# Kernel tuning notes

Hardware: AMD Instinct MI355X
Metric: run time of the kernel (lower is better)

## Reference

```python
import jax, jax.numpy as jnp
import numpy as np

L, H, D_MODEL, FFN = 2, 8, 1024, 4096
HD = D_MODEL // H          # head size = 128
SCALE_BASE = 512           # XPOS scale_base
EPS = 1e-5                 # LayerNorm / GroupNorm eps (torch default)


def _layernorm(x, w, b):
    mu = x.mean(-1, keepdims=True)
    var = ((x - mu) ** 2).mean(-1, keepdims=True)
    return (x - mu) * jax.lax.rsqrt(var + EPS) * w + b


def _groupnorm(y, w, b):
    # GroupNorm(heads, v_dim) applied row-wise on (B*S, v_dim): normalize each head's HD slice.
    B, S, _ = y.shape
    yg = y.reshape(B, S, H, HD)
    mu = yg.mean(-1, keepdims=True)
    var = ((yg - mu) ** 2).mean(-1, keepdims=True)
    yn = ((yg - mu) * jax.lax.rsqrt(var + EPS)).reshape(B, S, H * HD)
    return yn * w + b


def _xpos_tables(S):
    # XPOS: scale = ((arange(0,HD,2)+0.4*HD)/(1.4*HD)) ** (pos/scale_base); sin/cos from fixed_pos_embedding(scale)
    scale_vec = (np.arange(0, HD, 2) + 0.4 * HD) / (1.4 * HD)            # (HD/2,)
    power = (np.arange(S, dtype=np.float64) / SCALE_BASE)[:, None]
    scale = scale_vec[None, :] ** power                                   # (S, HD/2)
    half = HD // 2
    inv_freq = 1.0 / (10000.0 ** (np.arange(half, dtype=np.float64) / half))
    ang = np.arange(S, dtype=np.float64)[:, None] * inv_freq[None, :]
    sin, cos = np.sin(ang), np.cos(ang)
    dup = lambda m: jnp.asarray(np.repeat(m, 2, axis=-1).astype(np.float32))  # duplicate_interleave -> (S, HD)
    return dup(sin * scale), dup(cos * scale), dup(sin / scale), dup(cos / scale)


def _rotate_every_two(x):
    x1, x2 = x[..., ::2], x[..., 1::2]
    return jnp.stack((-x2, x1), axis=-1).reshape(x.shape)


def _decay_mask(S):
    # gammas = 1 - exp(linspace(log(1/32), log(1/512), H)); D[h,n,m] = gamma_h^(n-m) * (n>=m)
    gammas = 1.0 - np.exp(np.linspace(np.log(1.0 / 32), np.log(1.0 / 512), H))
    n = np.arange(S)[:, None]
    m = np.arange(S)[None, :]
    diff = (n - m).astype(np.float64)
    D = np.where(n >= m, gammas[:, None, None] ** diff[None], 0.0)
    return jnp.asarray(D.astype(np.float32))  # (H, S, S)


def setup_inputs() -> dict:
    key = jax.random.key(0)
    ks = jax.random.split(key, 8)
    B, S = 2, 2048
    rn = lambda k, shape, s: jax.random.normal(k, shape, dtype=jnp.float32) * s
    return {
        "X": rn(ks[0], (B, S, D_MODEL), 1.0),
        "ln1_w": jnp.ones((L, D_MODEL), jnp.float32), "ln1_b": jnp.zeros((L, D_MODEL), jnp.float32),
        "ln2_w": jnp.ones((L, D_MODEL), jnp.float32), "ln2_b": jnp.zeros((L, D_MODEL), jnp.float32),
        "WQ": rn(ks[1], (L, H, D_MODEL, HD), 1.0 / D_MODEL),
        "WK": rn(ks[2], (L, H, D_MODEL, HD), 1.0 / D_MODEL),
        "WV": rn(ks[3], (L, H, D_MODEL, HD), 1.0 / D_MODEL),
        "gn_w": jnp.ones((L, D_MODEL), jnp.float32), "gn_b": jnp.zeros((L, D_MODEL), jnp.float32),
        "WG": rn(ks[4], (L, D_MODEL, D_MODEL), 1.0 / D_MODEL),
        "WO": rn(ks[5], (L, D_MODEL, D_MODEL), 1.0 / D_MODEL),
        "ffn_w1": rn(ks[6], (L, D_MODEL, FFN), 1.0 / np.sqrt(D_MODEL)),
        "ffn_b1": jnp.zeros((L, FFN), jnp.float32),
        "ffn_w2": rn(ks[7], (L, FFN, D_MODEL), 1.0 / np.sqrt(FFN)),
        "ffn_b2": jnp.zeros((L, D_MODEL), jnp.float32),
    }


def reference(X, ln1_w, ln1_b, ln2_w, ln2_b, WQ, WK, WV, gn_w, gn_b, WG, WO,
              ffn_w1, ffn_b1, ffn_w2, ffn_b2):
    B, S, _ = X.shape
    sinq, cosq, sink, cosk = _xpos_tables(S)   # (S, HD) each; K uses downscale (1/scale)
    Dm = _decay_mask(S)                         # (H, S, S)
    for i in range(L):
        Xn = _layernorm(X, ln1_w[i], ln1_b[i])
        Q = jnp.einsum('bsd,hdk->bhsk', Xn, WQ[i])
        K = jnp.einsum('bsd,hdk->bhsk', Xn, WK[i])
        V = jnp.einsum('bsd,hdk->bhsk', Xn, WV[i])
        Q = Q * cosq + _rotate_every_two(Q) * sinq
        K = K * cosk + _rotate_every_two(K) * sink
        scores = jnp.einsum('bhsk,bhtk->bhst', Q, K) * Dm[None]  # decay-masked retention
        Yh = jnp.einsum('bhst,bhtk->bhsk', scores, V)
        Y = Yh.transpose(0, 2, 1, 3).reshape(B, S, H * HD)        # concat heads
        Y = _groupnorm(Y, gn_w[i], gn_b[i])
        G = jax.nn.silu(Xn @ WG[i])                               # swish gate on layernormed input
        Y = (G * Y) @ WO[i] + X                                   # retention + residual
        Yn = _layernorm(Y, ln2_w[i], ln2_b[i])
        X = jax.nn.silu(Yn @ ffn_w1[i] + ffn_b1[i]) @ ffn_w2[i] + ffn_b2[i] + Y
    return X
```

## Files before the change

kernel.cpp:

```cpp
#include <hip/hip_runtime.h>
#include <cstdint>
#include <cstddef>

#define LN_ 2
#define HH 8
#define DM 1024
#define FFN_ 4096
#define HDD 128
#define SS 2048
#define BB 2
#define RR (BB*SS)

typedef __bf16 bf16x8 __attribute__((ext_vector_type(8)));
typedef __bf16 bf16x4 __attribute__((ext_vector_type(4)));
typedef __bf16 bf16x2 __attribute__((ext_vector_type(2)));
typedef float  f32x4  __attribute__((ext_vector_type(4)));

__device__ __forceinline__ float silu_f(float x) { return x / (1.0f + expf(-x)); }

__device__ __forceinline__ void glds16(const void* g, void* l) {
  __builtin_amdgcn_global_load_lds(
      (const __attribute__((address_space(1))) unsigned int*)g,
      (__attribute__((address_space(3))) unsigned int*)l, 16, 0, 0);
}


__global__ void init_tables_k(float* __restrict__ sq, float* __restrict__ cq,
                              float* __restrict__ sk, float* __restrict__ ck,
                              float* __restrict__ lg2g) {
  int s = blockIdx.x, k = threadIdx.x;
  int j = k >> 1;
  double sv    = (2.0 * j + 0.4 * HDD) / (1.4 * HDD);
  double p     = (double)s / 512.0;
  double scale = pow(sv, p);
  double invf  = pow(10000.0, -((double)j) / 64.0);
  double ang   = (double)s * invf;
  double sn = sin(ang), cs = cos(ang);
  size_t idx = (size_t)s * HDD + k;
  sq[idx] = (float)(sn * scale);
  cq[idx] = (float)(cs * scale);
  sk[idx] = (float)(sn / scale);
  ck[idx] = (float)(cs / scale);
  if (s == 0 && k < HH) {
    double a0 = log(1.0 / 32.0), a1 = log(1.0 / 512.0);
    double x = a0 + (a1 - a0) * ((double)k / 7.0);
    lg2g[k] = (float)(log(1.0 - exp(x)) / log(2.0));
  }
}

__global__ __launch_bounds__(256) void ln_pack_k(
    const float* __restrict__ X, const float* __restrict__ w,
    const float* __restrict__ b, char* __restrict__ ph, char* __restrict__ pl) {
  const int row = blockIdx.x, tid = threadIdx.x;
  const float* x = X + (size_t)row * DM;
  float4 v = *(const float4*)(x + tid * 4);
  float s = v.x + v.y + v.z + v.w;
  float q = v.x * v.x + v.y * v.y + v.z * v.z + v.w * v.w;
#pragma unroll
  for (int o = 32; o > 0; o >>= 1) { s += __shfl_xor(s, o); q += __shfl_xor(q, o); }
  __shared__ float ss[4], qq[4];
  if ((tid & 63) == 0) { ss[tid >> 6] = s; qq[tid >> 6] = q; }
  __syncthreads();
  float S  = ss[0] + ss[1] + ss[2] + ss[3];
  float Qs = qq[0] + qq[1] + qq[2] + qq[3];
  float mu  = S * (1.0f / DM);
  float var = Qs * (1.0f / DM) - mu * mu;
  float rs  = 1.0f / sqrtf(var + 1e-5f);
  float4 wv = *(const float4*)(w + tid * 4);
  float4 bv = *(const float4*)(b + tid * 4);
  float y[4];
  y[0] = (v.x - mu) * rs * wv.x + bv.x;
  y[1] = (v.y - mu) * rs * wv.y + bv.y;
  y[2] = (v.z - mu) * rs * wv.z + bv.z;
  y[3] = (v.w - mu) * rs * wv.w + bv.w;
  bf16x4 hv, lv;
#pragma unroll
  for (int r = 0; r < 4; ++r) {
    __bf16 h = (__bf16)y[r];
    hv[r] = h;
    lv[r] = (__bf16)(y[r] - (float)h);
  }
  size_t tb = ((size_t)(row >> 7) * (DM / 64) + (tid >> 4)) * 16384;
  int off = (row & 127) * 128 + (((tid & 15) * 8) ^ ((row & 7) << 4));
  *(bf16x4*)(ph + tb + off) = hv;
  *(bf16x4*)(pl + tb + off) = lv;
}

__global__ __launch_bounds__(256) void packw_k(
    const float* __restrict__ W, char* __restrict__ dh, char* __restrict__ dl,
    int N, int qkv) {
  const int tn = blockIdx.x, tk = blockIdx.y, nkt = gridDim.y;
  __shared__ float L[64][132];
  const int k0 = tk * 64;
  const size_t srcbase = qkv ? ((size_t)tn * 131072 + (size_t)k0 * 128)
                             : ((size_t)k0 * N + (size_t)tn * 128);
  const int rstr = qkv ? 128 : N;
#pragma unroll
  for (int it = 0; it < 8; ++it) {
    int q = threadIdx.x + it * 256;
    int kk = q >> 5, c4 = (q & 31) * 4;
    float4 v = *(const float4*)(W + srcbase + (size_t)kk * rstr + c4);
    *(float4*)&L[kk][c4] = v;
  }
  __syncthreads();
  const size_t tb = ((size_t)tn * nkt + tk) * 16384;
#pragma unroll
  for (int it = 0; it < 4; ++it) {
    int o = threadIdx.x + it * 256;
    int n = o >> 3, k8 = o & 7;
    bf16x8 hv, lv;
#pragma unroll
    for (int j = 0; j < 8; ++j) {
      float x = L[k8 * 8 + j][n];
      __bf16 h = (__bf16)x;
      hv[j] = h;
      lv[j] = (__bf16)(x - (float)h);
    }
    int off = n * 128 + ((k8 * 16) ^ ((n & 7) << 4));
    *(bf16x8*)(dh + tb + off) = hv;
    *(bf16x8*)(dl + tb + off) = lv;
  }
}

__global__ __launch_bounds__(256) void vtpack_k(
    const float* __restrict__ V, char* __restrict__ dh, char* __restrict__ dl) {
  const int st = blockIdx.x, bh = blockIdx.y;
  __shared__ float L[64][132];
  const float* src = V + ((size_t)bh * SS + st * 64) * HDD;
#pragma unroll
  for (int it = 0; it < 8; ++it) {
    int q = threadIdx.x + it * 256;
    int r = q >> 5, c4 = (q & 31) * 4;
    *(float4*)&L[r][c4] = *(const float4*)(src + (size_t)r * HDD + c4);
  }
  __syncthreads();
  const size_t tb = ((size_t)bh * 32 + st) * 16384;
#pragma unroll
  for (int it = 0; it < 4; ++it) {
    int o = threadIdx.x + it * 256;
    int d = o >> 3, s8 = o & 7;
    bf16x8 hv, lv;
#pragma unroll
    for (int j = 0; j < 8; ++j) {
      float x = L[s8 * 8 + j][d];
      __bf16 h = (__bf16)x;
      hv[j] = h;
      lv[j] = (__bf16)(x - (float)h);
    }
    int off = d * 128 + ((s8 * 16) ^ ((d & 7) << 4));
    *(bf16x8*)(dh + tb + off) = hv;
    *(bf16x8*)(dl + tb + off) = lv;
  }
}

template <int MODE>
__global__ __launch_bounds__(256, 1) void mgemm_k(
    const char* __restrict__ pAh, const char* __restrict__ pAl,
    const char* __restrict__ pBh, const char* __restrict__ pBl,
    float* __restrict__ C, const float* __restrict__ bias,
    const float* __restrict__ resid, char* __restrict__ outH,
    char* __restrict__ outL, const float* __restrict__ tsin,
    const float* __restrict__ tcos, int M, int N, int K) {
  __shared__ char lds[2][4][16384];
  const int tid = threadIdx.x, lane = tid & 63, w = tid >> 6;
  const int wm = w & 1, wn = w >> 1;
  const int bx = blockIdx.x, by = blockIdx.y;
  const int nkt = K >> 6;
  const size_t tileA0 = (size_t)by * nkt * 16384;
  const size_t tileB0 = (size_t)bx * nkt * 16384;
  const int swz = (lane & 7) << 4;
  const int l15 = lane & 15, l4 = lane >> 4;

  f32x4 acc[4][4];
#pragma unroll
  for (int i = 0; i < 4; ++i)
#pragma unroll
    for (int j = 0; j < 4; ++j) acc[i][j] = (f32x4){0.f, 0.f, 0.f, 0.f};

  auto stage = [&](int buf, int t) {
    const size_t oA = tileA0 + (size_t)t * 16384;
    const size_t oB = tileB0 + (size_t)t * 16384;
#pragma unroll
    for (int c = 0; c < 4; ++c) {
      const size_t go = (size_t)c * 4096 + w * 1024 + lane * 16;
      const int lo = c * 4096 + w * 1024;
      glds16(pAh + oA + go, &lds[buf][0][lo]);
      glds16(pAl + oA + go, &lds[buf][1][lo]);
      glds16(pBh + oB + go, &lds[buf][2][lo]);
      glds16(pBl + oB + go, &lds[buf][3][lo]);
    }
  };

  auto comp = [&](int buf) {
#pragma unroll
    for (int ks = 0; ks < 2; ++ks) {
      const int kb = ks * 64 + l4 * 16;
      bf16x8 amh[4], aml[4], anh[4], anl[4];
#pragma unroll
      for (int f = 0; f < 4; ++f) {
        const int rm = wm * 64 + f * 16 + l15;
        const int ra = rm * 128 + (kb ^ swz);
        amh[f] = *(const bf16x8*)&lds[buf][0][ra];
        aml[f] = *(const bf16x8*)&lds[buf][1][ra];
        const int rn = wn * 64 + f * 16 + l15;
        const int rb = rn * 128 + (kb ^ swz);
        anh[f] = *(const bf16x8*)&lds[buf][2][rb];
        anl[f] = *(const bf16x8*)&lds[buf][3][rb];
      }
#pragma unroll
      for (int nf = 0; nf < 4; ++nf)
#pragma unroll
        for (int mf = 0; mf < 4; ++mf) {
          acc[nf][mf] = __builtin_amdgcn_mfma_f32_16x16x32_bf16(
              anh[nf], amh[mf], acc[nf][mf], 0, 0, 0);
          acc[nf][mf] = __builtin_amdgcn_mfma_f32_16x16x32_bf16(
              anh[nf], aml[mf], acc[nf][mf], 0, 0, 0);
          acc[nf][mf] = __builtin_amdgcn_mfma_f32_16x16x32_bf16(
              anl[nf], amh[mf], acc[nf][mf], 0, 0, 0);
        }
    }
  };

  stage(0, 0);
  __syncthreads();
  int buf = 0;
  for (int t = 0; t < nkt - 1; ++t) {
    stage(buf ^ 1, t + 1);
    comp(buf);
    __syncthreads();
    buf ^= 1;
  }
  comp(buf);

  const int mBase = by * 128 + wm * 64 + l15;
  const int nBase = bx * 128 + wn * 64 + l4 * 4;
#pragma unroll
  for (int nf = 0; nf < 4; ++nf)
#pragma unroll
    for (int mf = 0; mf < 4; ++mf) {
      const int m = mBase + mf * 16;
      const int n = nBase + nf * 16;
      f32x4 v = acc[nf][mf];
      if (MODE == 0) {
        *(f32x4*)(C + (((size_t)(m >> 11) * HH + (n >> 7)) * SS + (m & (SS - 1)))
                          * HDD + (n & (HDD - 1))) = v;
      } else if (MODE == 1) {
#pragma unroll
        for (int r = 0; r < 4; ++r) v[r] = silu_f(v[r]);
        *(f32x4*)(C + (size_t)m * N + n) = v;
      } else if (MODE == 2) {
        f32x4 rz = *(const f32x4*)(resid + (size_t)m * N + n);
        v += rz;
        *(f32x4*)(C + (size_t)m * N + n) = v;
      } else if (MODE == 3) {
        f32x4 bz = *(const f32x4*)(bias + n);
        bf16x4 hv, lv;
#pragma unroll
        for (int r = 0; r < 4; ++r) {
          float y = silu_f(v[r] + bz[r]);
          __bf16 h = (__bf16)y;
          hv[r] = h;
          lv[r] = (__bf16)(y - (float)h);
        }
        size_t tb = ((size_t)(m >> 7) * (N >> 6) + (n >> 6)) * 16384;
        int off = (m & 127) * 128 + (((n & 63) * 2) ^ ((m & 7) << 4));
        *(bf16x4*)(outH + tb + off) = hv;
        *(bf16x4*)(outL + tb + off) = lv;
      } else if (MODE == 4) {
        f32x4 bz = *(const f32x4*)(bias + n);
        f32x4 rz = *(const f32x4*)(resid + (size_t)m * N + n);
        v += bz + rz;
        *(f32x4*)(C + (size_t)m * N + n) = v;
      } else {
        int s = m & (SS - 1);
        int d = n & (HDD - 1);
        f32x4 sn = *(const f32x4*)(tsin + (size_t)s * HDD + d);
        f32x4 cn = *(const f32x4*)(tcos + (size_t)s * HDD + d);
        float o0 = v[0] * cn[0] - v[1] * sn[0];
        float o1 = v[1] * cn[1] + v[0] * sn[1];
        float o2 = v[2] * cn[2] - v[3] * sn[2];
        float o3 = v[3] * cn[3] + v[2] * sn[3];
        float oo[4] = {o0, o1, o2, o3};
        bf16x4 hv, lv;
#pragma unroll
        for (int r = 0; r < 4; ++r) {
          __bf16 h = (__bf16)oo[r];
          hv[r] = h;
          lv[r] = (__bf16)(oo[r] - (float)h);
        }
        size_t tile = ((size_t)(m >> 11) * HH + (n >> 7)) * 32 + (s >> 7) * 2 + (d >> 6);
        size_t off = tile * 16384 + (s & 127) * 128 + (((d & 63) * 2) ^ ((s & 7) << 4));
        *(bf16x4*)(outH + off) = hv;
        *(bf16x4*)(outL + off) = lv;
      }
    }
}

__global__ __launch_bounds__(256, 2) void mattn_k(
    const char* __restrict__ pQh, const char* __restrict__ pQl,
    const char* __restrict__ pKh, const char* __restrict__ pKl,
    const char* __restrict__ pVh, const char* __restrict__ pVl,
    const float* __restrict__ lg2g, float* __restrict__ Y) {
  __shared__ char Kls[2][2][8192];
  __shared__ char Vls[2][16384];
  __shared__ char Pls[2][8192];
  const int qt = 31 - blockIdx.x;
  const int bh = blockIdx.y;
  const int tid = threadIdx.x, lane = tid & 63, w = tid >> 6;
  const int wn = w & 1, wq = w >> 1;
  const int l15 = lane & 15, lg = lane >> 4;
  const float lg2 = lg2g[bh & 7];
  const size_t tb0 = (size_t)bh * 32;
  const int n0 = qt * 64;
  const int nt = qt + 1;

  bf16x8 qh[2][4], ql[2][4];
#pragma unroll
  for (int nf = 0; nf < 2; ++nf) {
    int rr = n0 + wn * 32 + nf * 16 + l15;
    size_t rowbase = (tb0 + (size_t)(rr >> 7) * 2) * 16384 + (size_t)(rr & 127) * 128;
    int sw = (rr & 7) << 4;
#pragma unroll
    for (int ks = 0; ks < 4; ++ks) {
      int d = ks * 32 + lg * 8;
      size_t a = rowbase + (size_t)(d >> 6) * 16384 + (((d & 63) * 2) ^ sw);
      qh[nf][ks] = *(const bf16x8*)(pQh + a);
      ql[nf][ks] = *(const bf16x8*)(pQl + a);
    }
  }

  f32x4 yacc[2][4];
#pragma unroll
  for (int i = 0; i < 2; ++i)
#pragma unroll
    for (int j = 0; j < 4; ++j) yacc[i][j] = (f32x4){0.f, 0.f, 0.f, 0.f};

  auto stageK = [&](int mt) {
    size_t half = (size_t)(mt & 1) * 8192;
#pragma unroll
    for (int dt = 0; dt < 2; ++dt) {
      size_t tile = (tb0 + (size_t)(mt >> 1) * 2 + dt) * 16384 + half;
#pragma unroll
      for (int c = 0; c < 2; ++c) {
        size_t go = (size_t)c * 4096 + w * 1024 + lane * 16;
        glds16(pKh + tile + go, &Kls[dt][0][c * 4096 + w * 1024]);
        glds16(pKl + tile + go, &Kls[dt][1][c * 4096 + w * 1024]);
      }
    }
  };
  auto stageV = [&](int mt) {
    size_t tile = (tb0 + mt) * 16384;
#pragma unroll
    for (int c = 0; c < 4; ++c) {
      size_t go = (size_t)c * 4096 + w * 1024 + lane * 16;
      glds16(pVh + tile + go, &Vls[0][c * 4096 + w * 1024]);
      glds16(pVl + tile + go, &Vls[1][c * 4096 + w * 1024]);
    }
  };

  stageK(0);
  stageV(0);
  __syncthreads();

  for (int mt = 0; mt < nt; ++mt) {
    f32x4 sacc[2][2];
#pragma unroll
    for (int i = 0; i < 2; ++i)
#pragma unroll
      for (int j = 0; j < 2; ++j) sacc[i][j] = (f32x4){0.f, 0.f, 0.f, 0.f};
#pragma unroll
    for (int ks = 0; ks < 4; ++ks) {
      int d = ks * 32 + lg * 8;
      bf16x8 kh[2], kl[2];
#pragma unroll
      for (int mf = 0; mf < 2; ++mf) {
        int m = wq * 32 + mf * 16 + l15;
        int off = (m & 63) * 128 + (((d & 63) * 2) ^ ((m & 7) << 4));
        kh[mf] = *(const bf16x8*)&Kls[d >> 6][0][off];
        kl[mf] = *(const bf16x8*)&Kls[d >> 6][1][off];
      }
#pragma unroll
      for (int nf = 0; nf < 2; ++nf)
#pragma unroll
        for (int mf = 0; mf < 2; ++mf) {
          sacc[nf][mf] = __builtin_amdgcn_mfma_f32_16x16x32_bf16(
              qh[nf][ks], kh[mf], sacc[nf][mf], 0, 0, 0);
          sacc[nf][mf] = __builtin_amdgcn_mfma_f32_16x16x32_bf16(
              qh[nf][ks], kl[mf], sacc[nf][mf], 0, 0, 0);
          sacc[nf][mf] = __builtin_amdgcn_mfma_f32_16x16x32_bf16(
              ql[nf][ks], kh[mf], sacc[nf][mf], 0, 0, 0);
        }
    }
    asm volatile("s_barrier" ::: "memory");
    if (mt + 1 < nt) stageK(mt + 1);

#pragma unroll
    for (int nf = 0; nf < 2; ++nf)
#pragma unroll
      for (int mf = 0; mf < 2; ++mf)
#pragma unroll
        for (int r = 0; r < 4; ++r) {
          int nl = wn * 32 + nf * 16 + lg * 4 + r;
          int ml = wq * 32 + mf * 16 + l15;
          int diff = (n0 + nl) - (mt * 64 + ml);
          float dec = (diff >= 0) ? exp2f((float)diff * lg2) : 0.0f;
          float p = sacc[nf][mf][r] * dec;
          __bf16 h = (__bf16)p;
          int off = nl * 128 + ((ml * 2) ^ ((nl & 7) << 4));
          *(__bf16*)&Pls[0][off] = h;
          *(__bf16*)&Pls[1][off] = (__bf16)(p - (float)h);
        }
    asm volatile("s_waitcnt lgkmcnt(0)" ::: "memory");
    asm volatile("s_barrier" ::: "memory");

#pragma unroll
    for (int ks = 0; ks < 2; ++ks) {
      int mchunk = ks * 32 + lg * 8;
      bf16x8 ph[2], pl2[2], vh[4], vl2[4];
#pragma unroll
      for (int nf = 0; nf < 2; ++nf) {
        int nl = wn * 32 + nf * 16 + l15;
        int off = nl * 128 + ((mchunk * 2) ^ ((nl & 7) << 4));
        ph[nf]  = *(const bf16x8*)&Pls[0][off];
        pl2[nf] = *(const bf16x8*)&Pls[1][off];
      }
#pragma unroll
      for (int df = 0; df < 4; ++df) {
        int d = wq * 64 + df * 16 + l15;
        int off = d * 128 + ((mchunk * 2) ^ ((d & 7) << 4));
        vh[df]  = *(const bf16x8*)&Vls[0][off];
        vl2[df] = *(const bf16x8*)&Vls[1][off];
      }
#pragma unroll
      for (int nf = 0; nf < 2; ++nf)
#pragma unroll
        for (int df = 0; df < 4; ++df) {
          yacc[nf][df] = __builtin_amdgcn_mfma_f32_16x16x32_bf16(
              ph[nf], vh[df], yacc[nf][df], 0, 0, 0);
          yacc[nf][df] = __builtin_amdgcn_mfma_f32_16x16x32_bf16(
              ph[nf], vl2[df], yacc[nf][df], 0, 0, 0);
          yacc[nf][df] = __builtin_amdgcn_mfma_f32_16x16x32_bf16(
              pl2[nf], vh[df], yacc[nf][df], 0, 0, 0);
        }
    }
    asm volatile("s_barrier" ::: "memory");
    if (mt + 1 < nt) stageV(mt + 1);
    __syncthreads();
  }

  const size_t yrow0 = (size_t)(bh >> 3) * SS + n0;
  const int hcol = (bh & 7) * HDD;
#pragma unroll
  for (int nf = 0; nf < 2; ++nf)
#pragma unroll
    for (int df = 0; df < 4; ++df)
#pragma unroll
      for (int r = 0; r < 4; ++r) {
        int nl = wn * 32 + nf * 16 + lg * 4 + r;
        int d  = wq * 64 + df * 16 + l15;
        Y[(yrow0 + nl) * DM + hcol + d] = yacc[nf][df][r];
      }
}

__global__ __launch_bounds__(256) void gn_gate_k(
    const float* __restrict__ Y, const float* __restrict__ w,
    const float* __restrict__ b, const float* __restrict__ G,
    char* __restrict__ ph, char* __restrict__ pl) {
  int g    = blockIdx.x * 4 + (threadIdx.x >> 6);
  int lane = threadIdx.x & 63;
  float2 v = *(const float2*)(Y + (size_t)g * HDD + lane * 2);
  float s = v.x + v.y, q = v.x * v.x + v.y * v.y;
#pragma unroll
  for (int o = 32; o > 0; o >>= 1) { s += __shfl_xor(s, o); q += __shfl_xor(q, o); }
  float mu  = s * (1.0f / HDD);
  float var = q * (1.0f / HDD) - mu * mu;
  float rs  = 1.0f / sqrtf(var + 1e-5f);
  int m   = g >> 3;
  int col = (g & 7) * HDD + lane * 2;
  float2 wv = *(const float2*)(w + col);
  float2 bv = *(const float2*)(b + col);
  float2 gv = *(const float2*)(G + (size_t)g * HDD + lane * 2);
  float ox = ((v.x - mu) * rs * wv.x + bv.x) * gv.x;
  float oy = ((v.y - mu) * rs * wv.y + bv.y) * gv.y;
  __bf16 hx = (__bf16)ox, hy = (__bf16)oy;
  bf16x2 hv, lv;
  hv[0] = hx; hv[1] = hy;
  lv[0] = (__bf16)(ox - (float)hx); lv[1] = (__bf16)(oy - (float)hy);
  size_t tb = ((size_t)(m >> 7) * (DM / 64) + (col >> 6)) * 16384;
  int off = (m & 127) * 128 + (((col & 63) * 2) ^ ((m & 7) << 4));
  *(bf16x2*)(ph + tb + off) = hv;
  *(bf16x2*)(pl + tb + off) = lv;
}

extern "C" void kernel_launch(void* const* d_in, const int* in_sizes, int n_in,
                              void* d_out, int out_size, void* d_ws, size_t ws_size,
                              hipStream_t stream) {
  (void)in_sizes; (void)n_in; (void)out_size; (void)ws_size;
  const float* X0   = (const float*)d_in[0];
  const float* ln1w = (const float*)d_in[1];
  const float* ln1b = (const float*)d_in[2];
  const float* ln2w = (const float*)d_in[3];
  const float* ln2b = (const float*)d_in[4];
  const float* WQ   = (const float*)d_in[5];
  const float* WK   = (const float*)d_in[6];
  const float* WV   = (const float*)d_in[7];
  const float* gnw  = (const float*)d_in[8];
  const float* gnb  = (const float*)d_in[9];
  const float* WG   = (const float*)d_in[10];
  const float* WO   = (const float*)d_in[11];
  const float* W1   = (const float*)d_in[12];
  const float* B1   = (const float*)d_in[13];
  const float* W2   = (const float*)d_in[14];
  const float* B2   = (const float*)d_in[15];

  char* wsb = (char*)d_ws;
  const size_t MB = 1 << 20;
  float* bufA = (float*)(wsb + 0 * MB);
  float* bufB = (float*)(wsb + 16 * MB);
  float* bufE = (float*)(wsb + 32 * MB);
  float* bufF = (float*)(wsb + 48 * MB);
  float* bufG = (float*)(wsb + 64 * MB);
  float* sq   = (float*)(wsb + 80 * MB);
  float* cq   = (float*)(wsb + 81 * MB);
  float* sk   = (float*)(wsb + 82 * MB);
  float* ck   = (float*)(wsb + 83 * MB);
  float* lg2g = (float*)(wsb + 84 * MB);
  char* pXh = wsb + 85 * MB;
  char* pXl = wsb + 93 * MB;
  char* pWh = wsb + 101 * MB;
  char* pWl = wsb + 127 * MB;
  char* R   = wsb + 153 * MB;
  char* pFh = R;
  char* pFl = R + 32 * MB;
  char* pQh = R;
  char* pQl = R + 8 * MB;
  char* pKh = R + 16 * MB;
  char* pKl = R + 24 * MB;
  char* pVh = R + 32 * MB;
  char* pVl = R + 40 * MB;
  const size_t oWQ = 0, oWK = (size_t)2 << 20, oWV = (size_t)4 << 20,
               oWG = (size_t)6 << 20, oWO = (size_t)8 << 20,
               oW1 = (size_t)10 << 20, oW2 = (size_t)18 << 20;

  init_tables_k<<<SS, HDD, 0, stream>>>(sq, cq, sk, ck, lg2g);

  const dim3 g1(8, 32);
  const dim3 gF1(32, 32);
  for (int i = 0; i < LN_; ++i) {
    const float* Xin = (i == 0) ? X0 : bufA;
    packw_k<<<dim3(8, 16), 256, 0, stream>>>(WQ + (size_t)i * 1048576, pWh + oWQ, pWl + oWQ, 1024, 1);
    packw_k<<<dim3(8, 16), 256, 0, stream>>>(WK + (size_t)i * 1048576, pWh + oWK, pWl + oWK, 1024, 1);
    packw_k<<<dim3(8, 16), 256, 0, stream>>>(WV + (size_t)i * 1048576, pWh + oWV, pWl + oWV, 1024, 1);
    packw_k<<<dim3(8, 16), 256, 0, stream>>>(WG + (size_t)i * 1048576, pWh + oWG, pWl + oWG, 1024, 0);
    packw_k<<<dim3(8, 16), 256, 0, stream>>>(WO + (size_t)i * 1048576, pWh + oWO, pWl + oWO, 1024, 0);
    packw_k<<<dim3(32, 16), 256, 0, stream>>>(W1 + (size_t)i * 4194304, pWh + oW1, pWl + oW1, 4096, 0);
    packw_k<<<dim3(8, 64), 256, 0, stream>>>(W2 + (size_t)i * 4194304, pWh + oW2, pWl + oW2, 1024, 0);

    ln_pack_k<<<RR, 256, 0, stream>>>(Xin, ln1w + i * DM, ln1b + i * DM, pXh, pXl);
    mgemm_k<5><<<g1, 256, 0, stream>>>(pXh, pXl, pWh + oWQ, pWl + oWQ, nullptr,
                                       nullptr, nullptr, pQh, pQl, sq, cq, RR, DM, DM);
    mgemm_k<5><<<g1, 256, 0, stream>>>(pXh, pXl, pWh + oWK, pWl + oWK, nullptr,
                                       nullptr, nullptr, pKh, pKl, sk, ck, RR, DM, DM);
    mgemm_k<0><<<g1, 256, 0, stream>>>(pXh, pXl, pWh + oWV, pWl + oWV, bufE,
                                       nullptr, nullptr, nullptr, nullptr, nullptr, nullptr, RR, DM, DM);
    mgemm_k<1><<<g1, 256, 0, stream>>>(pXh, pXl, pWh + oWG, pWl + oWG, bufF,
                                       nullptr, nullptr, nullptr, nullptr, nullptr, nullptr, RR, DM, DM);
    vtpack_k<<<dim3(32, 16), 256, 0, stream>>>(bufE, pVh, pVl);
    mattn_k<<<dim3(32, 16), 256, 0, stream>>>(pQh, pQl, pKh, pKl, pVh, pVl, lg2g, bufG);
    gn_gate_k<<<RR * HH / 4, 256, 0, stream>>>(bufG, gnw + i * DM, gnb + i * DM,
                                               bufF, pXh, pXl);
    mgemm_k<2><<<g1, 256, 0, stream>>>(pXh, pXl, pWh + oWO, pWl + oWO, bufB,
                                       nullptr, Xin, nullptr, nullptr, nullptr, nullptr, RR, DM, DM);
    ln_pack_k<<<RR, 256, 0, stream>>>(bufB, ln2w + i * DM, ln2b + i * DM, pXh, pXl);
    mgemm_k<3><<<gF1, 256, 0, stream>>>(pXh, pXl, pWh + oW1, pWl + oW1, nullptr,
                                        B1 + (size_t)i * FFN_, nullptr, pFh, pFl,
                                        nullptr, nullptr, RR, FFN_, DM);
    float* Xout = (i == LN_ - 1) ? (float*)d_out : bufA;
    mgemm_k<4><<<g1, 256, 0, stream>>>(pFh, pFl, pWh + oW2, pWl + oW2, Xout,
                                       B2 + (size_t)i * DM, bufB, nullptr, nullptr,
                                       nullptr, nullptr, RR, DM, FFN_);
  }
}
```

Before: 1.302 ms.

## Fuse QKVG projections into one launch, single-buffer GEMM, narrow N tiles

Merges the four Q/K/V/G projection GEMMs into one kernel launch with a z-dimension that picks the weight slice and epilogue. The GEMM main loop drops LDS double-buffering in favour of a single buffer synchronised each step, which cuts LDS use so more blocks can be resident per CU. The N=1024 output GEMMs now use 128x64 tiles (NF=2) to double the grid and reach 3 blocks per CU. In exchange, global-load latency is no longer hidden by in-block prefetch and has to be covered by occupancy instead.

```diff
diff --git a/kernel.cpp b/kernel.cpp
--- a/kernel.cpp
+++ b/kernel.cpp
@@ -153,62 +153,53 @@
   }
 }
 
-template <int MODE>
-__global__ __launch_bounds__(256, 1) void mgemm_k(
+template <int NF>
+__device__ __forceinline__ void gemm_main(
     const char* __restrict__ pAh, const char* __restrict__ pAl,
     const char* __restrict__ pBh, const char* __restrict__ pBl,
-    float* __restrict__ C, const float* __restrict__ bias,
-    const float* __restrict__ resid, char* __restrict__ outH,
-    char* __restrict__ outL, const float* __restrict__ tsin,
-    const float* __restrict__ tcos, int M, int N, int K) {
-  __shared__ char lds[2][4][16384];
+    size_t tA0, size_t tB0, int nkt, char* lds, f32x4 (&acc)[NF][4]) {
   const int tid = threadIdx.x, lane = tid & 63, w = tid >> 6;
   const int wm = w & 1, wn = w >> 1;
-  const int bx = blockIdx.x, by = blockIdx.y;
-  const int nkt = K >> 6;
-  const size_t tileA0 = (size_t)by * nkt * 16384;
-  const size_t tileB0 = (size_t)bx * nkt * 16384;
   const int swz = (lane & 7) << 4;
   const int l15 = lane & 15, l4 = lane >> 4;
-
-  f32x4 acc[4][4];
-#pragma unroll
-  for (int i = 0; i < 4; ++i)
-#pragma unroll
-    for (int j = 0; j < 4; ++j) acc[i][j] = (f32x4){0.f, 0.f, 0.f, 0.f};
-
-  auto stage = [&](int buf, int t) {
-    const size_t oA = tileA0 + (size_t)t * 16384;
-    const size_t oB = tileB0 + (size_t)t * 16384;
+  char* lAh = lds;
+  char* lAl = lds + 16384;
+  char* lBh = lds + 32768;
+  char* lBl = lds + 32768 + NF * 4096;
+  for (int t = 0; t < nkt; ++t) {
+    const size_t oA = tA0 + (size_t)t * 16384;
+    const size_t oB = tB0 + (size_t)t * 16384;
 #pragma unroll
     for (int c = 0; c < 4; ++c) {
       const size_t go = (size_t)c * 4096 + w * 1024 + lane * 16;
-      const int lo = c * 4096 + w * 1024;
-      glds16(pAh + oA + go, &lds[buf][0][lo]);
-      glds16(pAl + oA + go, &lds[buf][1][lo]);
-      glds16(pBh + oB + go, &lds[buf][2][lo]);
-      glds16(pBl + oB + go, &lds[buf][3][lo]);
-    }
-  };
-
-  auto comp = [&](int buf) {
+      glds16(pAh + oA + go, lAh + c * 4096 + w * 1024);
+      glds16(pAl + oA + go, lAl + c * 4096 + w * 1024);
+    }
+#pragma unroll
+    for (int c = 0; c < NF; ++c) {
+      const size_t go = (size_t)c * 4096 + w * 1024 + lane * 16;
+      glds16(pBh + oB + go, lBh + c * 4096 + w * 1024);
+      glds16(pBl + oB + go, lBl + c * 4096 + w * 1024);
+    }
+    __syncthreads();
 #pragma unroll
     for (int ks = 0; ks < 2; ++ks) {
       const int kb = ks * 64 + l4 * 16;
-      bf16x8 amh[4], aml[4], anh[4], anl[4];
+      bf16x8 amh[4], aml[4], anh[NF], anl[NF];
 #pragma unroll
       for (int f = 0; f < 4; ++f) {
-        const int rm = wm * 64 + f * 16 + l15;
-        const int ra = rm * 128 + (kb ^ swz);
-        amh[f] = *(const bf16x8*)&lds[buf][0][ra];
-        aml[f] = *(const bf16x8*)&lds[buf][1][ra];
-        const int rn = wn * 64 + f * 16 + l15;
-        const int rb = rn * 128 + (kb ^ swz);
-        anh[f] = *(const bf16x8*)&lds[buf][2][rb];
-        anl[f] = *(const bf16x8*)&lds[buf][3][rb];
-      }
-#pragma unroll
-      for (int nf = 0; nf < 4; ++nf)
+        const int ra = (wm * 64 + f * 16 + l15) * 128 + (kb ^ swz);
+        amh[f] = *(const bf16x8*)&lAh[ra];
+        aml[f] = *(const bf16x8*)&lAl[ra];
+      }
+#pragma unroll
+      for (int f = 0; f < NF; ++f) {
+        const int rb = (wn * (NF * 16) + f * 16 + l15) * 128 + (kb ^ swz);
+        anh[f] = *(const bf16x8*)&lBh[rb];
+        anl[f] = *(const bf16x8*)&lBl[rb];
+      }
+#pragma unroll
+      for (int nf = 0; nf < NF; ++nf)
 #pragma unroll
         for (int mf = 0; mf < 4; ++mf) {
           acc[nf][mf] = __builtin_amdgcn_mfma_f32_16x16x32_bf16(
@@ -219,36 +210,44 @@
               anl[nf], amh[mf], acc[nf][mf], 0, 0, 0);
         }
     }
-  };
-
-  stage(0, 0);
-  __syncthreads();
-  int buf = 0;
-  for (int t = 0; t < nkt - 1; ++t) {
-    stage(buf ^ 1, t + 1);
-    comp(buf);
     __syncthreads();
-    buf ^= 1;
-  }
-  comp(buf);
+  }
+}
+
+template <int MODE, int NF>
+__global__ __launch_bounds__(256, (NF == 2 ? 3 : 2)) void mgemm_k(
+    const char* __restrict__ pAh, const char* __restrict__ pAl,
+    const char* __restrict__ pBh, const char* __restrict__ pBl,
+    float* __restrict__ C, const float* __restrict__ bias,
+    const float* __restrict__ resid, char* __restrict__ outH,
+    char* __restrict__ outL, int N, int K) {
+  __shared__ char lds[32768 + NF * 8192];
+  const int lane = threadIdx.x & 63, w = threadIdx.x >> 6;
+  const int wm = w & 1, wn = w >> 1;
+  const int l15 = lane & 15, l4 = lane >> 4;
+  const int bx = blockIdx.x, by = blockIdx.y;
+  const int nkt = K >> 6;
+  const size_t tA0 = (size_t)by * nkt * 16384;
+  const size_t tB0 = (NF == 4) ? (size_t)bx * nkt * 16384
+                               : (size_t)(bx >> 1) * nkt * 16384 + (size_t)(bx & 1) * 8192;
+  f32x4 acc[NF][4];
+#pragma unroll
+  for (int i = 0; i < NF; ++i)
+#pragma unroll
+    for (int j = 0; j < 4; ++j) acc[i][j] = (f32x4){0.f, 0.f, 0.f, 0.f};
+
+  gemm_main<NF>(pAh, pAl, pBh, pBl, tA0, tB0, nkt, lds, acc);
 
   const int mBase = by * 128 + wm * 64 + l15;
-  const int nBase = bx * 128 + wn * 64 + l4 * 4;
-#pragma unroll
-  for (int nf = 0; nf < 4; ++nf)
+  const int nBase = bx * (NF * 32) + wn * (NF * 16) + l4 * 4;
+#pragma unroll
+  for (int nf = 0; nf < NF; ++nf)
 #pragma unroll
     for (int mf = 0; mf < 4; ++mf) {
       const int m = mBase + mf * 16;
       const int n = nBase + nf * 16;
       f32x4 v = acc[nf][mf];
-      if (MODE == 0) {
-        *(f32x4*)(C + (((size_t)(m >> 11) * HH + (n >> 7)) * SS + (m & (SS - 1)))
-                          * HDD + (n & (HDD - 1))) = v;
-      } else if (MODE == 1) {
-#pragma unroll
-        for (int r = 0; r < 4; ++r) v[r] = silu_f(v[r]);
-        *(f32x4*)(C + (size_t)m * N + n) = v;
-      } else if (MODE == 2) {
+      if (MODE == 2) {
         f32x4 rz = *(const f32x4*)(resid + (size_t)m * N + n);
         v += rz;
         *(f32x4*)(C + (size_t)m * N + n) = v;
@@ -266,16 +265,65 @@
         int off = (m & 127) * 128 + (((n & 63) * 2) ^ ((m & 7) << 4));
         *(bf16x4*)(outH + tb + off) = hv;
         *(bf16x4*)(outL + tb + off) = lv;
-      } else if (MODE == 4) {
+      } else {
         f32x4 bz = *(const f32x4*)(bias + n);
         f32x4 rz = *(const f32x4*)(resid + (size_t)m * N + n);
         v += bz + rz;
         *(f32x4*)(C + (size_t)m * N + n) = v;
+      }
+    }
+}
+
+__global__ __launch_bounds__(256, 2) void qkvg_k(
+    const char* __restrict__ pXh, const char* __restrict__ pXl,
+    const char* __restrict__ pWh, const char* __restrict__ pWl,
+    float* __restrict__ V, float* __restrict__ G,
+    char* __restrict__ pQh, char* __restrict__ pQl,
+    char* __restrict__ pKh, char* __restrict__ pKl,
+    const float* __restrict__ sq, const float* __restrict__ cq,
+    const float* __restrict__ sk, const float* __restrict__ ck) {
+  __shared__ char lds[65536];
+  const int lane = threadIdx.x & 63, w = threadIdx.x >> 6;
+  const int wm = w & 1, wn = w >> 1;
+  const int l15 = lane & 15, l4 = lane >> 4;
+  const int bx = blockIdx.x, by = blockIdx.y, z = blockIdx.z;
+  const int nkt = DM >> 6;
+  const size_t tA0 = (size_t)by * nkt * 16384;
+  const size_t tB0 = (size_t)bx * nkt * 16384;
+  const size_t wo = (size_t)z << 21;
+  f32x4 acc[4][4];
+#pragma unroll
+  for (int i = 0; i < 4; ++i)
+#pragma unroll
+    for (int j = 0; j < 4; ++j) acc[i][j] = (f32x4){0.f, 0.f, 0.f, 0.f};
+
+  gemm_main<4>(pXh, pXl, pWh + wo, pWl + wo, tA0, tB0, nkt, lds, acc);
+
+  const int mBase = by * 128 + wm * 64 + l15;
+  const int nBase = bx * 128 + wn * 64 + l4 * 4;
+#pragma unroll
+  for (int nf = 0; nf < 4; ++nf)
+#pragma unroll
+    for (int mf = 0; mf < 4; ++mf) {
+      const int m = mBase + mf * 16;
+      const int n = nBase + nf * 16;
+      f32x4 v = acc[nf][mf];
+      if (z == 2) {
+        *(f32x4*)(V + (((size_t)(m >> 11) * HH + (n >> 7)) * SS + (m & (SS - 1)))
+                          * HDD + (n & (HDD - 1))) = v;
+      } else if (z == 3) {
+#pragma unroll
+        for (int r = 0; r < 4; ++r) v[r] = silu_f(v[r]);
+        *(f32x4*)(G + (size_t)m * DM + n) = v;
       } else {
+        const float* tsn = (z == 0) ? sq : sk;
+        const float* tcs = (z == 0) ? cq : ck;
+        char* oh = (z == 0) ? pQh : pKh;
+        char* ol = (z == 0) ? pQl : pKl;
         int s = m & (SS - 1);
         int d = n & (HDD - 1);
-        f32x4 sn = *(const f32x4*)(tsin + (size_t)s * HDD + d);
-        f32x4 cn = *(const f32x4*)(tcos + (size_t)s * HDD + d);
+        f32x4 sn = *(const f32x4*)(tsn + (size_t)s * HDD + d);
+        f32x4 cn = *(const f32x4*)(tcs + (size_t)s * HDD + d);
         float o0 = v[0] * cn[0] - v[1] * sn[0];
         float o1 = v[1] * cn[1] + v[0] * sn[1];
         float o2 = v[2] * cn[2] - v[3] * sn[2];
@@ -290,8 +338,8 @@
         }
         size_t tile = ((size_t)(m >> 11) * HH + (n >> 7)) * 32 + (s >> 7) * 2 + (d >> 6);
         size_t off = tile * 16384 + (s & 127) * 128 + (((d & 63) * 2) ^ ((s & 7) << 4));
-        *(bf16x4*)(outH + off) = hv;
-        *(bf16x4*)(outL + off) = lv;
+        *(bf16x4*)(oh + off) = hv;
+        *(bf16x4*)(ol + off) = lv;
       }
     }
 }
@@ -538,46 +586,38 @@
   char* pKl = R + 24 * MB;
   char* pVh = R + 32 * MB;
   char* pVl = R + 40 * MB;
-  const size_t oWQ = 0, oWK = (size_t)2 << 20, oWV = (size_t)4 << 20,
-               oWG = (size_t)6 << 20, oWO = (size_t)8 << 20,
-               oW1 = (size_t)10 << 20, oW2 = (size_t)18 << 20;
+  const size_t oWQ = 0, oW1 = (size_t)10 << 20, oWO = (size_t)8 << 20,
+               oW2 = (size_t)18 << 20;
 
   init_tables_k<<<SS, HDD, 0, stream>>>(sq, cq, sk, ck, lg2g);
 
-  const dim3 g1(8, 32);
-  const dim3 gF1(32, 32);
   for (int i = 0; i < LN_; ++i) {
     const float* Xin = (i == 0) ? X0 : bufA;
     packw_k<<<dim3(8, 16), 256, 0, stream>>>(WQ + (size_t)i * 1048576, pWh + oWQ, pWl + oWQ, 1024, 1);
-    packw_k<<<dim3(8, 16), 256, 0, stream>>>(WK + (size_t)i * 1048576, pWh + oWK, pWl + oWK, 1024, 1);
-    packw_k<<<dim3(8, 16), 256, 0, stream>>>(WV + (size_t)i * 1048576, pWh + oWV, pWl + oWV, 1024, 1);
-    packw_k<<<dim3(8, 16), 256, 0, stream>>>(WG + (size_t)i * 1048576, pWh + oWG, pWl + oWG, 1024, 0);
+    packw_k<<<dim3(8, 16), 256, 0, stream>>>(WK + (size_t)i * 1048576, pWh + 2 * MB, pWl + 2 * MB, 1024, 1);
+    packw_k<<<dim3(8, 16), 256, 0, stream>>>(WV + (size_t)i * 1048576, pWh + 4 * MB, pWl + 4 * MB, 1024, 1);
+    packw_k<<<dim3(8, 16), 256, 0, stream>>>(WG + (size_t)i * 1048576, pWh + 6 * MB, pWl + 6 * MB, 1024, 0);
     packw_k<<<dim3(8, 16), 256, 0, stream>>>(WO + (size_t)i * 1048576, pWh + oWO, pWl + oWO, 1024, 0);
     packw_k<<<dim3(32, 16), 256, 0, stream>>>(W1 + (size_t)i * 4194304, pWh + oW1, pWl + oW1, 4096, 0);
     packw_k<<<dim3(8, 64), 256, 0, stream>>>(W2 + (size_t)i * 4194304, pWh + oW2, pWl + oW2, 1024, 0);
 
     ln_pack_k<<<RR, 256, 0, stream>>>(Xin, ln1w + i * DM, ln1b + i * DM, pXh, pXl);
-    mgemm_k<5><<<g1, 256, 0, stream>>>(pXh, pXl, pWh + oWQ, pWl + oWQ, nullptr,
-                                       nullptr, nullptr, pQh, pQl, sq, cq, RR, DM, DM);
-    mgemm_k<5><<<g1, 256, 0, stream>>>(pXh, pXl, pWh + oWK, pWl + oWK, nullptr,
-                                       nullptr, nullptr, pKh, pKl, sk, ck, RR, DM, DM);
-    mgemm_k<0><<<g1, 256, 0, stream>>>(pXh, pXl, pWh + oWV, pWl + oWV, bufE,
-                                       nullptr, nullptr, nullptr, nullptr, nullptr, nullptr, RR, DM, DM);
-    mgemm_k<1><<<g1, 256, 0, stream>>>(pXh, pXl, pWh + oWG, pWl + oWG, bufF,
-                                       nullptr, nullptr, nullptr, nullptr, nullptr, nullptr, RR, DM, DM);
+    qkvg_k<<<dim3(8, 32, 4), 256, 0, stream>>>(pXh, pXl, pWh, pWl, bufE, bufF,
+                                               pQh, pQl, pKh, pKl, sq, cq, sk, ck);
     vtpack_k<<<dim3(32, 16), 256, 0, stream>>>(bufE, pVh, pVl);
     mattn_k<<<dim3(32, 16), 256, 0, stream>>>(pQh, pQl, pKh, pKl, pVh, pVl, lg2g, bufG);
     gn_gate_k<<<RR * HH / 4, 256, 0, stream>>>(bufG, gnw + i * DM, gnb + i * DM,
                                                bufF, pXh, pXl);
-    mgemm_k<2><<<g1, 256, 0, stream>>>(pXh, pXl, pWh + oWO, pWl + oWO, bufB,
-                                       nullptr, Xin, nullptr, nullptr, nullptr, nullptr, RR, DM, DM);
+    mgemm_k<2, 2><<<dim3(16, 32), 256, 0, stream>>>(pXh, pXl, pWh + oWO, pWl + oWO,
+                                                    bufB, nullptr, Xin, nullptr, nullptr,
+                                                    DM, DM);
     ln_pack_k<<<RR, 256, 0, stream>>>(bufB, ln2w + i * DM, ln2b + i * DM, pXh, pXl);
-    mgemm_k<3><<<gF1, 256, 0, stream>>>(pXh, pXl, pWh + oW1, pWl + oW1, nullptr,
-                                        B1 + (size_t)i * FFN_, nullptr, pFh, pFl,
-                                        nullptr, nullptr, RR, FFN_, DM);
+    mgemm_k<3, 4><<<dim3(32, 32), 256, 0, stream>>>(pXh, pXl, pWh + oW1, pWl + oW1,
+                                                    nullptr, B1 + (size_t)i * FFN_,
+                                                    nullptr, pFh, pFl, FFN_, DM);
     float* Xout = (i == LN_ - 1) ? (float*)d_out : bufA;
-    mgemm_k<4><<<g1, 256, 0, stream>>>(pFh, pFl, pWh + oW2, pWl + oW2, Xout,
-                                       B2 + (size_t)i * DM, bufB, nullptr, nullptr,
-                                       nullptr, nullptr, RR, DM, FFN_);
-  }
-}
+    mgemm_k<4, 2><<<dim3(16, 32), 256, 0, stream>>>(pFh, pFl, pWh + oW2, pWl + oW2,
+                                                    Xout, B2 + (size_t)i * DM, bufB,
+                                                    nullptr, nullptr, DM, FFN_);
+  }
+}
```

Result: faster. 1.191 ms (-8.5%).
